# Optimization experiments

Hardware: AMD Instinct MI355X
Metric: run time of the kernel (lower is better)

## Reference

```python
import jax, jax.numpy as jnp
import numpy as np

B, S, H, D = 4, 1024, 16, 64


def setup_inputs() -> dict:
    key = jax.random.key(0)
    k1, k2 = jax.random.split(key)
    qkv = jax.random.normal(k1, (B, S, 3, H, D), dtype=jnp.float32)
    bias = jax.random.normal(k2, (1, H, S, S), dtype=jnp.float32)
    return {"qkv": qkv, "bias": bias}


def reference(qkv, bias):
    # flash_attn_qkvpacked_func(qkv, softmax_scale=None -> 1/sqrt(D), bias=bias, causal=False)
    q = qkv[:, :, 0]  # (B, S, H, D)
    k = qkv[:, :, 1]
    v = qkv[:, :, 2]
    scale = 1.0 / jnp.sqrt(jnp.asarray(D, dtype=qkv.dtype))
    # scores: (B, H, S_q, S_k)
    scores = jnp.einsum("bshd,bthd->bhst", q, k) * scale + bias
    probs = jax.nn.softmax(scores, axis=-1)
    out = jnp.einsum("bhst,bthd->bshd", probs, v)  # (B, S, H, D)
    return out
```

## Files before the change

### kernel.cpp

```cpp
#include <hip/hip_runtime.h>

#define NB 4
#define NS 1024
#define NH 16
#define ND 64

typedef __attribute__((ext_vector_type(8))) short bf16x8;
typedef __attribute__((ext_vector_type(4))) float f32x4;

static __device__ __forceinline__ short f2bf(float x) {
  __bf16 h = (__bf16)x;
  return __builtin_bit_cast(short, h);
}
static __device__ __forceinline__ float bf2f(short s) {
  unsigned u = ((unsigned)(unsigned short)s) << 16;
  return __builtin_bit_cast(float, u);
}

__global__ __launch_bounds__(512, 2)
void fsa_fwd(const float* __restrict__ qkv,
             const float* __restrict__ bias,
             float* __restrict__ out)
{
  const int hw = blockIdx.x;
  const int lg = ((hw & 7) << 6) | (hw >> 3);
  const int b  = lg & 3;
  const int qt = (lg >> 2) & 7;
  const int h  = lg >> 5;

  const int tid  = threadIdx.x;
  const int w    = tid >> 6;
  const int lane = tid & 63;
  const int lo   = lane & 15;
  const int hi   = lane >> 4;
  const int q0   = qt * 128;

  __shared__ __attribute__((aligned(16))) short Ksh[64 * 64];
  __shared__ __attribute__((aligned(16))) short VTsh[64 * 64];
  __shared__ __attribute__((aligned(16))) short Psh[8][16 * 64];

  bf16x8 qf[2];
  {
    const int qs = q0 + w * 16 + lo;
    const float* qp = qkv + ((size_t)(b * NS + qs) * 3) * (NH * ND) + h * ND + hi * 8;
    #pragma unroll
    for (int f = 0; f < 2; ++f) {
      float4 x0 = *(const float4*)(qp + f * 32);
      float4 x1 = *(const float4*)(qp + f * 32 + 4);
      float v[8] = {x0.x, x0.y, x0.z, x0.w, x1.x, x1.y, x1.z, x1.w};
      #pragma unroll
      for (int j = 0; j < 8; ++j) qf[f][j] = f2bf(v[j] * 0.125f);
    }
  }

  const size_t tstr = 3 * NH * ND;
  const float* kg = qkv + (size_t)b * NS * tstr + 1 * NH * ND + h * ND;
  const float* vg = qkv + (size_t)b * NS * tstr + 2 * NH * ND + h * ND;

  const int krow = tid >> 3;
  const int kd   = (tid & 7) * 8;
  const int vrow = (tid & 31) * 2;
  const int vd   = (tid >> 5) * 4;

  const float* bb = bias + (size_t)h * NS * NS + (size_t)(q0 + w * 16 + hi * 4) * NS + lo;

  float psum[4] = {0.f, 0.f, 0.f, 0.f};
  f32x4 oacc[4];
  #pragma unroll
  for (int dt = 0; dt < 4; ++dt) { f32x4 z = {0.f, 0.f, 0.f, 0.f}; oacc[dt] = z; }

  for (int it = 0; it < 16; ++it) {
    const int t0 = it * 64;

    bf16x8 w0;
    {
      const float* src = kg + (size_t)(t0 + krow) * tstr + kd;
      float4 a = ((const float4*)src)[0];
      float4 c = ((const float4*)src)[1];
      float v[8] = {a.x,a.y,a.z,a.w, c.x,c.y,c.z,c.w};
      #pragma unroll
      for (int j = 0; j < 8; ++j) w0[j] = f2bf(v[j]);
    }
    unsigned vpk[4];
    {
      const float* s0 = vg + (size_t)(t0 + vrow) * tstr + vd;
      const float* s1 = s0 + tstr;
      float4 a0 = *(const float4*)s0;
      float4 b0 = *(const float4*)s1;
      float r0[4] = {a0.x,a0.y,a0.z,a0.w};
      float r1[4] = {b0.x,b0.y,b0.z,b0.w};
      #pragma unroll
      for (int j = 0; j < 4; ++j)
        vpk[j] = (unsigned)(unsigned short)f2bf(r0[j]) |
                 ((unsigned)(unsigned short)f2bf(r1[j]) << 16);
    }

    __syncthreads();

    {
      const int base = krow * 64 + kd;
      const int sw = (krow & 7) << 3;
      *(bf16x8*)&Ksh[(base ^ sw)] = w0;
    }
    {
      unsigned* vt32 = (unsigned*)VTsh;
      #pragma unroll
      for (int j = 0; j < 4; ++j) {
        const int R = vd + j;
        vt32[R * 32 + ((vrow >> 1) ^ ((R & 7) << 2))] = vpk[j];
      }
    }

    float br[4][4];
    #pragma unroll
    for (int r = 0; r < 4; ++r)
      #pragma unroll
      for (int tt = 0; tt < 4; ++tt)
        br[r][tt] = bb[(size_t)r * NS + t0 + tt * 16];

    __syncthreads();

    __builtin_amdgcn_s_setprio(1);
    f32x4 sacc[4];
    #pragma unroll
    for (int tt = 0; tt < 4; ++tt) {
      f32x4 sb;
      #pragma unroll
      for (int r = 0; r < 4; ++r) sb[r] = br[r][tt] - 8.f;
      const int kr = tt * 16 + lo;
      const int ksw = (kr & 7) << 3;
      bf16x8 k0 = *(const bf16x8*)&Ksh[(kr * 64      + hi * 8) ^ ksw];
      bf16x8 k1 = *(const bf16x8*)&Ksh[(kr * 64 + 32 + hi * 8) ^ ksw];
      sb = __builtin_amdgcn_mfma_f32_16x16x32_bf16(qf[0], k0, sb, 0, 0, 0);
      sb = __builtin_amdgcn_mfma_f32_16x16x32_bf16(qf[1], k1, sb, 0, 0, 0);
      sacc[tt] = sb;
    }

    short* pw = Psh[w];
    #pragma unroll
    for (int r = 0; r < 4; ++r) {
      const int row = hi * 4 + r;
      const int sw = (row & 7) << 3;
      #pragma unroll
      for (int tt = 0; tt < 4; ++tt) {
        float p = __expf(sacc[tt][r]);
        short pb = f2bf(p);
        psum[r] += bf2f(pb);
        pw[row * 64 + ((tt * 16 + lo) ^ sw)] = pb;
      }
    }
    asm volatile("s_waitcnt lgkmcnt(0)" ::: "memory");

    bf16x8 pf0, pf1;
    {
      const int psw = (lo & 7) << 3;
      pf0 = *(const bf16x8*)&pw[lo * 64 + ((     hi * 8) ^ psw)];
      pf1 = *(const bf16x8*)&pw[lo * 64 + ((32 + hi * 8) ^ psw)];
    }
    #pragma unroll
    for (int dt = 0; dt < 4; ++dt) {
      const int vr = dt * 16 + lo;
      const int vsw = (vr & 7) << 3;
      bf16x8 v0 = *(const bf16x8*)&VTsh[vr * 64 + ((     hi * 8) ^ vsw)];
      bf16x8 v1 = *(const bf16x8*)&VTsh[vr * 64 + ((32 + hi * 8) ^ vsw)];
      oacc[dt] = __builtin_amdgcn_mfma_f32_16x16x32_bf16(pf0, v0, oacc[dt], 0, 0, 0);
      oacc[dt] = __builtin_amdgcn_mfma_f32_16x16x32_bf16(pf1, v1, oacc[dt], 0, 0, 0);
    }
    __builtin_amdgcn_s_setprio(0);
  }

  #pragma unroll
  for (int r = 0; r < 4; ++r) {
    psum[r] += __shfl_xor(psum[r], 1, 64);
    psum[r] += __shfl_xor(psum[r], 2, 64);
    psum[r] += __shfl_xor(psum[r], 4, 64);
    psum[r] += __shfl_xor(psum[r], 8, 64);
  }

  float* ob = out + ((size_t)(b * NS + q0 + w * 16 + hi * 4) * NH + h) * ND + lo;
  #pragma unroll
  for (int r = 0; r < 4; ++r) {
    float inv = 1.f / psum[r];
    #pragma unroll
    for (int dt = 0; dt < 4; ++dt)
      ob[(size_t)r * NH * ND + dt * 16] = oacc[dt][r] * inv;
  }
}

extern "C" void kernel_launch(void* const* d_in, const int* in_sizes, int n_in,
                              void* d_out, int out_size, void* d_ws, size_t ws_size,
                              hipStream_t stream) {
  const float* qkv  = (const float*)d_in[0];
  const float* bias = (const float*)d_in[1];
  float* out = (float*)d_out;
  dim3 grid(NB * NH * (NS / 128));
  fsa_fwd<<<grid, 512, 0, stream>>>(qkv, bias, out);
}
```

Before: 49.22 us.

## Double-buffer K/V tiles in LDS and drop one barrier per iteration

K and V shared tiles are duplicated so the next tile is loaded, converted and stored into the alternate buffer while the current tile is used for QK and PV MFMAs. This removes one of the two __syncthreads per iteration and is meant to overlap global load latency with compute. It doubles the K/V LDS footprint and puts the staging stores before the compute, which may still stall on the global loads.

```diff
diff --git a/kernel.cpp b/kernel.cpp
--- a/kernel.cpp
+++ b/kernel.cpp
@@ -35,8 +35,8 @@
   const int hi   = lane >> 4;
   const int q0   = qt * 128;
 
-  __shared__ __attribute__((aligned(16))) short Ksh[64 * 64];
-  __shared__ __attribute__((aligned(16))) short VTsh[64 * 64];
+  __shared__ __attribute__((aligned(16))) short Ksh[2][64 * 64];
+  __shared__ __attribute__((aligned(16))) short VTsh[2][64 * 64];
   __shared__ __attribute__((aligned(16))) short Psh[8][16 * 64];
 
   bf16x8 qf[2];
@@ -69,47 +69,53 @@
   #pragma unroll
   for (int dt = 0; dt < 4; ++dt) { f32x4 z = {0.f, 0.f, 0.f, 0.f}; oacc[dt] = z; }
 
+#define STAGE(T0, BUF) do { \
+    bf16x8 w0_; \
+    { \
+      const float* src_ = kg + (size_t)((T0) + krow) * tstr + kd; \
+      float4 a_ = ((const float4*)src_)[0]; \
+      float4 c_ = ((const float4*)src_)[1]; \
+      float v_[8] = {a_.x,a_.y,a_.z,a_.w, c_.x,c_.y,c_.z,c_.w}; \
+      _Pragma("unroll") \
+      for (int j_ = 0; j_ < 8; ++j_) w0_[j_] = f2bf(v_[j_]); \
+    } \
+    unsigned vpk_[4]; \
+    { \
+      const float* s0_ = vg + (size_t)((T0) + vrow) * tstr + vd; \
+      const float* s1_ = s0_ + tstr; \
+      float4 a0_ = *(const float4*)s0_; \
+      float4 b0_ = *(const float4*)s1_; \
+      float r0_[4] = {a0_.x,a0_.y,a0_.z,a0_.w}; \
+      float r1_[4] = {b0_.x,b0_.y,b0_.z,b0_.w}; \
+      _Pragma("unroll") \
+      for (int j_ = 0; j_ < 4; ++j_) \
+        vpk_[j_] = (unsigned)(unsigned short)f2bf(r0_[j_]) | \
+                   ((unsigned)(unsigned short)f2bf(r1_[j_]) << 16); \
+    } \
+    { \
+      const int base_ = krow * 64 + kd; \
+      const int sw_ = (krow & 7) << 3; \
+      *(bf16x8*)&Ksh[BUF][base_ ^ sw_] = w0_; \
+    } \
+    { \
+      unsigned* vt_ = (unsigned*)VTsh[BUF]; \
+      _Pragma("unroll") \
+      for (int j_ = 0; j_ < 4; ++j_) { \
+        const int R_ = vd + j_; \
+        vt_[R_ * 32 + ((vrow >> 1) ^ ((R_ & 7) << 2))] = vpk_[j_]; \
+      } \
+    } \
+  } while (0)
+
+  STAGE(0, 0);
+  __syncthreads();
+
+  #pragma unroll 1
   for (int it = 0; it < 16; ++it) {
+    const int cur = it & 1;
     const int t0 = it * 64;
 
-    bf16x8 w0;
-    {
-      const float* src = kg + (size_t)(t0 + krow) * tstr + kd;
-      float4 a = ((const float4*)src)[0];
-      float4 c = ((const float4*)src)[1];
-      float v[8] = {a.x,a.y,a.z,a.w, c.x,c.y,c.z,c.w};
-      #pragma unroll
-      for (int j = 0; j < 8; ++j) w0[j] = f2bf(v[j]);
-    }
-    unsigned vpk[4];
-    {
-      const float* s0 = vg + (size_t)(t0 + vrow) * tstr + vd;
-      const float* s1 = s0 + tstr;
-      float4 a0 = *(const float4*)s0;
-      float4 b0 = *(const float4*)s1;
-      float r0[4] = {a0.x,a0.y,a0.z,a0.w};
-      float r1[4] = {b0.x,b0.y,b0.z,b0.w};
-      #pragma unroll
-      for (int j = 0; j < 4; ++j)
-        vpk[j] = (unsigned)(unsigned short)f2bf(r0[j]) |
-                 ((unsigned)(unsigned short)f2bf(r1[j]) << 16);
-    }
-
-    __syncthreads();
-
-    {
-      const int base = krow * 64 + kd;
-      const int sw = (krow & 7) << 3;
-      *(bf16x8*)&Ksh[(base ^ sw)] = w0;
-    }
-    {
-      unsigned* vt32 = (unsigned*)VTsh;
-      #pragma unroll
-      for (int j = 0; j < 4; ++j) {
-        const int R = vd + j;
-        vt32[R * 32 + ((vrow >> 1) ^ ((R & 7) << 2))] = vpk[j];
-      }
-    }
+    if (it < 15) STAGE(t0 + 64, cur ^ 1);
 
     float br[4][4];
     #pragma unroll
@@ -117,8 +123,6 @@
       #pragma unroll
       for (int tt = 0; tt < 4; ++tt)
         br[r][tt] = bb[(size_t)r * NS + t0 + tt * 16];
-
-    __syncthreads();
 
     __builtin_amdgcn_s_setprio(1);
     f32x4 sacc[4];
@@ -129,8 +133,8 @@
       for (int r = 0; r < 4; ++r) sb[r] = br[r][tt] - 8.f;
       const int kr = tt * 16 + lo;
       const int ksw = (kr & 7) << 3;
-      bf16x8 k0 = *(const bf16x8*)&Ksh[(kr * 64      + hi * 8) ^ ksw];
-      bf16x8 k1 = *(const bf16x8*)&Ksh[(kr * 64 + 32 + hi * 8) ^ ksw];
+      bf16x8 k0 = *(const bf16x8*)&Ksh[cur][(kr * 64      + hi * 8) ^ ksw];
+      bf16x8 k1 = *(const bf16x8*)&Ksh[cur][(kr * 64 + 32 + hi * 8) ^ ksw];
       sb = __builtin_amdgcn_mfma_f32_16x16x32_bf16(qf[0], k0, sb, 0, 0, 0);
       sb = __builtin_amdgcn_mfma_f32_16x16x32_bf16(qf[1], k1, sb, 0, 0, 0);
       sacc[tt] = sb;
@@ -161,13 +165,17 @@
     for (int dt = 0; dt < 4; ++dt) {
       const int vr = dt * 16 + lo;
       const int vsw = (vr & 7) << 3;
-      bf16x8 v0 = *(const bf16x8*)&VTsh[vr * 64 + ((     hi * 8) ^ vsw)];
-      bf16x8 v1 = *(const bf16x8*)&VTsh[vr * 64 + ((32 + hi * 8) ^ vsw)];
+      bf16x8 v0 = *(const bf16x8*)&VTsh[cur][vr * 64 + ((     hi * 8) ^ vsw)];
+      bf16x8 v1 = *(const bf16x8*)&VTsh[cur][vr * 64 + ((32 + hi * 8) ^ vsw)];
       oacc[dt] = __builtin_amdgcn_mfma_f32_16x16x32_bf16(pf0, v0, oacc[dt], 0, 0, 0);
       oacc[dt] = __builtin_amdgcn_mfma_f32_16x16x32_bf16(pf1, v1, oacc[dt], 0, 0, 0);
     }
     __builtin_amdgcn_s_setprio(0);
-  }
+
+    __syncthreads();
+  }
+
+#undef STAGE
 
   #pragma unroll
   for (int r = 0; r < 4; ++r) {
```

After: 51.37 us. +4.4%, slower.
